# Performance work log

Measured on AMD Instinct MI355X. Metric: run time of the kernel, lower is better.

## Reference

```python
import jax, jax.numpy as jnp
import numpy as np

N_NODES = 200000
AVG_DEG = 64
N_EDGES = N_NODES * AVG_DEG
ALPHA = 0.1
DT = 0.01
EPS = 1e-9
DIFF = 10.0
HARD_LO = -jnp.pi / 2
HARD_HI = jnp.pi / 2


def setup_inputs() -> dict:
    key = jax.random.key(0)
    ks = jax.random.split(key, 8)
    xy = jax.random.normal(ks[0], (N_NODES, 2), dtype=jnp.float32)
    xy_dot_old = jax.random.normal(ks[1], (N_NODES, 2), dtype=jnp.float32)
    scale = 2.0 * np.pi
    phase = (jax.random.uniform(ks[2], (N_NODES,), dtype=jnp.float32) * 2 - 1) * scale
    w = (jax.random.uniform(ks[3], (N_NODES,), dtype=jnp.float32) * 2 - 1) * scale
    amplitudes = (jax.random.uniform(ks[4], (N_NODES,), dtype=jnp.float32) * 2 - 1) * scale
    ha = jax.random.normal(ks[5], (N_NODES,), dtype=jnp.float32)
    edge_src = jnp.sort(jax.random.randint(ks[6], (N_EDGES,), 0, N_NODES, dtype=jnp.int32))
    edge_dst = jax.random.randint(ks[7], (N_EDGES,), 0, N_NODES, dtype=jnp.int32)
    return {
        "xy": xy,
        "xy_dot_old": xy_dot_old,
        "phase": phase,
        "w": w,
        "amplitudes": amplitudes,
        "ha": ha,
        "edge_src": edge_src,
        "edge_dst": edge_dst,
    }


def reference(xy, xy_dot_old, phase, w, amplitudes, ha, edge_src, edge_dst):
    n = xy.shape[0]
    x, y = xy[:, 0], xy[:, 1]
    xd_old, yd_old = xy_dot_old[:, 0], xy_dot_old[:, 1]

    # per-node gain matrix K_i = [[a, -b], [b, a]]
    r2 = x * x + y * y
    a = ALPHA * (1.0 - r2 * r2)                         # term_a
    zeta = 1.0 - ha * ((xd_old + EPS) / (jnp.abs(xd_old) + EPS))
    b = w / (zeta + EPS)                                # term_b
    kx = a * x - b * y                                  # (K_i @ xy_i).x
    ky = b * x + a * y                                  # (K_i @ xy_i).y

    # edge coupling: R(phase_i - phase_j) @ xy_j, summed over neighbors j of i
    pd = phase[edge_src] - phase[edge_dst]
    c, s = jnp.cos(pd), jnp.sin(pd)
    xj = x[edge_dst]
    yj = y[edge_dst]
    ex = c * xj - s * yj
    ey = s * xj + c * yj
    sum_x = jax.ops.segment_sum(ex, edge_src, num_segments=n)
    sum_y = jax.ops.segment_sum(ey, edge_src, num_segments=n)

    # integrate with rate clamp
    x_dot = jnp.clip(kx + sum_x, xd_old - DIFF, xd_old + DIFF)
    y_dot = jnp.clip(ky + sum_y, yd_old - DIFF, yd_old + DIFF)
    x_new = x + x_dot * DT
    y_new = y + y_dot * DT

    angles = jnp.clip(amplitudes * y_new, HARD_LO, HARD_HI)
    xy_new = jnp.stack([x_new, y_new], axis=-1)
    xy_dot_old_new = xy  # original sets xy_dot_old[i] = old xy[i]
    return angles, xy_new, xy_dot_old_new
```

## Files before the change

kernel.cpp:

```cpp
#include <hip/hip_runtime.h>
#include <math.h>
#include <limits.h>

#define ALPHA  0.1f
#define DT     0.01f
#define EPSV   1e-9f
#define DIFF   10.0f
#define HARD_P 1.5707963267948966f

typedef int v4i __attribute__((ext_vector_type(4)));

__global__ void node_pre(const float2* __restrict__ xy,
                         const float*  __restrict__ phase,
                         float2* __restrict__ g,
                         float2* __restrict__ out_xyold,
                         float2* __restrict__ Gsum,
                         int n) {
    int i = blockIdx.x * blockDim.x + threadIdx.x;
    if (i >= n) return;
    float2 p = xy[i];
    float ph = phase[i];
    float s, c;
    sincosf(ph, &s, &c);
    float2 gv;
    gv.x = p.x * c + p.y * s;
    gv.y = p.y * c - p.x * s;
    g[i] = gv;
    out_xyold[i] = p;
    float2 z; z.x = 0.f; z.y = 0.f;
    Gsum[i] = z;
}

__global__ __launch_bounds__(256) void edge_seg4(
        const int*    __restrict__ src,
        const int*    __restrict__ dst,
        const float2* __restrict__ g,
        float* __restrict__ Gsum,
        int n_edges) {
    const int lane = threadIdx.x & 63;
    const int wib  = threadIdx.x >> 6;
    const long wave = (long)blockIdx.x * 4 + wib;
    const long base = wave * 256 + (long)lane * 4;

    int   sk[4];
    float vx[4], vy[4];

    if (base + 3 < (long)n_edges) {
        v4i sv = __builtin_nontemporal_load((const v4i*)(src + base));
        v4i dv = __builtin_nontemporal_load((const v4i*)(dst + base));
        sk[0]=sv.x; sk[1]=sv.y; sk[2]=sv.z; sk[3]=sv.w;
        float2 g0 = g[dv.x];
        float2 g1 = g[dv.y];
        float2 g2 = g[dv.z];
        float2 g3 = g[dv.w];
        vx[0]=g0.x; vy[0]=g0.y; vx[1]=g1.x; vy[1]=g1.y;
        vx[2]=g2.x; vy[2]=g2.y; vx[3]=g3.x; vy[3]=g3.y;
    } else {
        #pragma unroll
        for (int j = 0; j < 4; ++j) {
            long e = base + j;
            if (e < (long)n_edges) {
                sk[j] = src[e];
                float2 gd = g[dst[e]];
                vx[j] = gd.x; vy[j] = gd.y;
            } else {
                sk[j] = INT_MAX;
                vx[j] = 0.f; vy[j] = 0.f;
            }
        }
    }

    int   kF = sk[0], rk = sk[0];
    float fx = 0.f, fy = 0.f;
    float rx = vx[0], ry = vy[0];
    bool  firstClosed = false;
    #pragma unroll
    for (int j = 1; j < 4; ++j) {
        if (sk[j] == rk) {
            rx += vx[j]; ry += vy[j];
        } else {
            if (!firstClosed) { fx = rx; fy = ry; firstClosed = true; }
            else {
                atomicAdd(&Gsum[2*rk],   rx);
                atomicAdd(&Gsum[2*rk+1], ry);
            }
            rk = sk[j]; rx = vx[j]; ry = vy[j];
        }
    }
    const int  kL   = rk;
    const bool pure = !firstClosed;

    float ax = rx, ay = ry;
    int   key = kL;
    #pragma unroll
    for (int off = 1; off < 64; off <<= 1) {
        float px = __shfl_up(ax, off);
        float py = __shfl_up(ay, off);
        int   pk = __shfl_up(key, off);
        if (lane >= off && pk == key) { ax += px; ay += py; }
    }

    float pscx = __shfl_up(ax, 1);
    float pscy = __shfl_up(ay, 1);
    int   pKL  = __shfl_up(key, 1);
    int   nKF  = __shfl_down(kF, 1);

    if (!pure) {
        float gx_ = fx, gy_ = fy;
        if (lane > 0 && pKL == kF) { gx_ += pscx; gy_ += pscy; }
        atomicAdd(&Gsum[2*kF],   gx_);
        atomicAdd(&Gsum[2*kF+1], gy_);
    }
    bool endHere = (lane == 63) || (nKF != key);
    if (key != INT_MAX && endHere) {
        atomicAdd(&Gsum[2*key],   ax);
        atomicAdd(&Gsum[2*key+1], ay);
    }
}

__global__ void node_post(const float2* __restrict__ xy,
                          const float2* __restrict__ xyd,
                          const float*  __restrict__ phase,
                          const float*  __restrict__ w,
                          const float*  __restrict__ amps,
                          const float*  __restrict__ ha,
                          const float2* __restrict__ Gsum,
                          float* __restrict__ out,
                          int n) {
    int i = blockIdx.x * blockDim.x + threadIdx.x;
    if (i >= n) return;
    float2 p   = xy[i];
    float2 pdv = xyd[i];
    float x = p.x, y = p.y;
    float xd = pdv.x, yd = pdv.y;

    float r2 = x*x + y*y;
    float a = ALPHA * (1.0f - r2*r2);
    float h = ha[i];
    float zeta = 1.0f - h * ((xd + EPSV) / (fabsf(xd) + EPSV));
    float b = w[i] / (zeta + EPSV);
    float kx = a*x - b*y;
    float ky = b*x + a*y;

    float2 gv = Gsum[i];
    float s, c;
    sincosf(phase[i], &s, &c);
    float sumx = c*gv.x - s*gv.y;
    float sumy = s*gv.x + c*gv.y;

    float xdot = fminf(fmaxf(kx + sumx, xd - DIFF), xd + DIFF);
    float ydot = fminf(fmaxf(ky + sumy, yd - DIFF), yd + DIFF);
    float xn = x + xdot * DT;
    float yn = y + ydot * DT;

    float ang = fminf(fmaxf(amps[i] * yn, -HARD_P), HARD_P);

    out[i] = ang;
    float2* xy_new = (float2*)(out + n);
    float2 v; v.x = xn; v.y = yn;
    xy_new[i] = v;
}

extern "C" void kernel_launch(void* const* d_in, const int* in_sizes, int n_in,
                              void* d_out, int out_size, void* d_ws, size_t ws_size,
                              hipStream_t stream) {
    const float2* xy    = (const float2*)d_in[0];
    const float2* xyd   = (const float2*)d_in[1];
    const float*  phase = (const float*)d_in[2];
    const float*  w     = (const float*)d_in[3];
    const float*  amps  = (const float*)d_in[4];
    const float*  ha    = (const float*)d_in[5];
    const int*    esrc  = (const int*)d_in[6];
    const int*    edst  = (const int*)d_in[7];

    const int n       = in_sizes[2];
    const int n_edges = in_sizes[6];

    float* out = (float*)d_out;

    float2* g    = (float2*)d_ws;
    float2* Gsum = (float2*)((char*)d_ws + (size_t)n * sizeof(float2));

    const int B = 256;
    node_pre<<<(n + B - 1) / B, B, 0, stream>>>(
        xy, phase, g, (float2*)(out + (size_t)3 * n), Gsum, n);

    int n_blocks = (n_edges + 1023) / 1024;
    edge_seg4<<<n_blocks, B, 0, stream>>>(esrc, edst, g, (float*)Gsum, n_edges);

    node_post<<<(n + B - 1) / B, B, 0, stream>>>(
        xy, xyd, phase, w, amps, ha, Gsum, out, n);
}
```

Before: 198.8 us.

## Use persistent waves with software-pipelined index loads and gathers, 8 edges per lane

The edge kernel becomes a persistent grid-stride loop over 512-edge tiles, capped at 1024 blocks. Each lane now handles 8 edges instead of 4, which enlarges the per-lane run-length merge. Index loads are prefetched two tiles ahead and gathers one tile ahead, so memory latency overlaps the segmented scan and atomics. The cost is more register pressure from the triple buffers and a fixed grid size that may underfill the GPU or lose occupancy.

```diff
diff --git a/kernel.cpp b/kernel.cpp
--- a/kernel.cpp
+++ b/kernel.cpp
@@ -31,43 +31,58 @@
     Gsum[i] = z;
 }
 
-__global__ __launch_bounds__(256) void edge_seg4(
-        const int*    __restrict__ src,
-        const int*    __restrict__ dst,
-        const float2* __restrict__ g,
-        float* __restrict__ Gsum,
-        int n_edges) {
-    const int lane = threadIdx.x & 63;
-    const int wib  = threadIdx.x >> 6;
-    const long wave = (long)blockIdx.x * 4 + wib;
-    const long base = wave * 256 + (long)lane * 4;
-
-    int   sk[4];
-    float vx[4], vy[4];
-
-    if (base + 3 < (long)n_edges) {
-        v4i sv = __builtin_nontemporal_load((const v4i*)(src + base));
-        v4i dv = __builtin_nontemporal_load((const v4i*)(dst + base));
-        sk[0]=sv.x; sk[1]=sv.y; sk[2]=sv.z; sk[3]=sv.w;
-        float2 g0 = g[dv.x];
-        float2 g1 = g[dv.y];
-        float2 g2 = g[dv.z];
-        float2 g3 = g[dv.w];
-        vx[0]=g0.x; vy[0]=g0.y; vx[1]=g1.x; vy[1]=g1.y;
-        vx[2]=g2.x; vy[2]=g2.y; vx[3]=g3.x; vy[3]=g3.y;
+#define EPL 8
+#define TILE_EDGES 512
+
+struct Idx8 { int s[EPL]; int d[EPL]; };
+
+__device__ __forceinline__ void load_idx(Idx8& I,
+                                         const int* __restrict__ src,
+                                         const int* __restrict__ dst,
+                                         long tile_base, int n_edges, int lane) {
+    long b = tile_base + (long)lane * EPL;
+    if (b + (EPL - 1) < (long)n_edges) {
+        v4i s0 = __builtin_nontemporal_load((const v4i*)(src + b));
+        v4i s1 = __builtin_nontemporal_load((const v4i*)(src + b + 4));
+        v4i d0 = __builtin_nontemporal_load((const v4i*)(dst + b));
+        v4i d1 = __builtin_nontemporal_load((const v4i*)(dst + b + 4));
+        #pragma unroll
+        for (int j = 0; j < 4; ++j) { I.s[j] = s0[j]; I.s[j + 4] = s1[j]; }
+        #pragma unroll
+        for (int j = 0; j < 4; ++j) { I.d[j] = d0[j]; I.d[j + 4] = d1[j]; }
     } else {
         #pragma unroll
-        for (int j = 0; j < 4; ++j) {
-            long e = base + j;
-            if (e < (long)n_edges) {
-                sk[j] = src[e];
-                float2 gd = g[dst[e]];
-                vx[j] = gd.x; vy[j] = gd.y;
-            } else {
-                sk[j] = INT_MAX;
-                vx[j] = 0.f; vy[j] = 0.f;
-            }
+        for (int j = 0; j < EPL; ++j) {
+            long e = b + j;
+            if (e < (long)n_edges) { I.s[j] = src[e]; I.d[j] = dst[e]; }
+            else                   { I.s[j] = INT_MAX; I.d[j] = 0; }
         }
+    }
+}
+
+__device__ __forceinline__ void gather_g(float gx[EPL], float gy[EPL],
+                                         const float2* __restrict__ g,
+                                         const Idx8& I) {
+    #pragma unroll
+    for (int j = 0; j < EPL; ++j) {
+        float2 v = g[I.d[j]];
+        gx[j] = v.x; gy[j] = v.y;
+    }
+}
+
+__device__ __forceinline__ void compute_tile(const Idx8& I,
+                                             const float gx[EPL],
+                                             const float gy[EPL],
+                                             float* __restrict__ Gsum,
+                                             int lane) {
+    int   sk[EPL];
+    float vx[EPL], vy[EPL];
+    #pragma unroll
+    for (int j = 0; j < EPL; ++j) {
+        sk[j] = I.s[j];
+        bool valid = (sk[j] != INT_MAX);
+        vx[j] = valid ? gx[j] : 0.f;
+        vy[j] = valid ? gy[j] : 0.f;
     }
 
     int   kF = sk[0], rk = sk[0];
@@ -75,7 +90,7 @@
     float rx = vx[0], ry = vy[0];
     bool  firstClosed = false;
     #pragma unroll
-    for (int j = 1; j < 4; ++j) {
+    for (int j = 1; j < EPL; ++j) {
         if (sk[j] == rk) {
             rx += vx[j]; ry += vy[j];
         } else {
@@ -115,6 +130,45 @@
     if (key != INT_MAX && endHere) {
         atomicAdd(&Gsum[2*key],   ax);
         atomicAdd(&Gsum[2*key+1], ay);
+    }
+}
+
+__global__ __launch_bounds__(256, 4) void edge_seg8(
+        const int*    __restrict__ src,
+        const int*    __restrict__ dst,
+        const float2* __restrict__ g,
+        float* __restrict__ Gsum,
+        int n_edges) {
+    const int lane   = threadIdx.x & 63;
+    const int wib    = threadIdx.x >> 6;
+    const int wave   = blockIdx.x * 4 + wib;
+    const int nwaves = gridDim.x * 4;
+    const int n_tiles = (n_edges + TILE_EDGES - 1) / TILE_EDGES;
+
+    int tc = wave;
+    if (tc >= n_tiles) return;
+
+    Idx8 A, B, C;
+    float gax[EPL], gay[EPL], gbx[EPL], gby[EPL];
+
+    load_idx(A, src, dst, (long)tc * TILE_EDGES, n_edges, lane);
+    gather_g(gax, gay, g, A);
+    int  tn   = tc + nwaves;
+    bool hasN = (tn < n_tiles);
+    if (hasN) load_idx(B, src, dst, (long)tn * TILE_EDGES, n_edges, lane);
+
+    for (;;) {
+        int  tn2   = tn + nwaves;
+        bool hasN2 = hasN && (tn2 < n_tiles);
+        if (hasN2) load_idx(C, src, dst, (long)tn2 * TILE_EDGES, n_edges, lane);
+        if (hasN)  gather_g(gbx, gby, g, B);
+        compute_tile(A, gax, gay, Gsum, lane);
+        if (!hasN) break;
+        A = B;
+        #pragma unroll
+        for (int j = 0; j < EPL; ++j) { gax[j] = gbx[j]; gay[j] = gby[j]; }
+        B = C;
+        tn = tn2; hasN = hasN2;
     }
 }
 
@@ -185,8 +239,11 @@
     node_pre<<<(n + B - 1) / B, B, 0, stream>>>(
         xy, phase, g, (float2*)(out + (size_t)3 * n), Gsum, n);
 
-    int n_blocks = (n_edges + 1023) / 1024;
-    edge_seg4<<<n_blocks, B, 0, stream>>>(esrc, edst, g, (float*)Gsum, n_edges);
+    int n_tiles = (n_edges + TILE_EDGES - 1) / TILE_EDGES;
+    int blocks  = (n_tiles + 3) / 4;
+    if (blocks > 1024) blocks = 1024;
+    if (blocks < 1)    blocks = 1;
+    edge_seg8<<<blocks, B, 0, stream>>>(esrc, edst, g, (float*)Gsum, n_edges);
 
     node_post<<<(n + B - 1) / B, B, 0, stream>>>(
         xy, xyd, phase, w, amps, ha, Gsum, out, n);
```

After: 198.0 us. About the same (-0.4%).
